# Kernel optimization log

Hardware: AMD Instinct MI355X
Metric: run time of the kernel (lower is better)

Reference implementation:

```python
import jax, jax.numpy as jnp
import numpy as np

# Config matching init_kwargs: input_shape=(C,T,H,W)=(512,32,14,14), window_size=9, n_heads=8
B, C, T, H, W = 2, 512, 32, 14, 14
N, K = 8, 9
CI = C // N              # per-head inter channels (64)
P = (K - 1) // 2         # symmetric temporal zero-pad so S == T


def setup_inputs() -> dict:
    key = jax.random.key(0)
    ks = jax.random.split(key, 7)
    s = 0.02
    return {
        "x":  jax.random.normal(ks[0], (B, C, T, H, W), jnp.float32),
        # per-head 1x1x1 conv (Linear3d) weights/biases, stacked over heads
        "Wq": jax.random.normal(ks[1], (N, CI, C), jnp.float32) * s,
        "bq": jax.random.normal(ks[2], (N, CI), jnp.float32) * s,
        "Wk": jax.random.normal(ks[3], (N, CI, C), jnp.float32) * s,
        "bk": jax.random.normal(ks[4], (N, CI), jnp.float32) * s,
        "Wv": jax.random.normal(ks[5], (N, CI, C), jnp.float32) * s,
        "bv": jax.random.normal(ks[6], (N, CI), jnp.float32) * s,
    }


def reference(x, Wq, bq, Wk, bk, Wv, bv):
    # x: (B, C, T, H, W). Dropout (p=0.25) is inference-mode identity.
    Bx, Cx, Tx, Hx, Wd = x.shape
    HW = Hx * Wd
    xf = x.reshape(Bx, Cx, Tx, HW)

    # Queries: every original frame is the center of its own window -> project x directly.
    q = jnp.einsum('bctp,nic->bnitp', xf, Wq) + bq[None, :, :, None, None]  # (B,N,ci,T,HW)

    # Keys/values on temporally zero-padded input (Pad3d gives S == T windows).
    xp = jnp.pad(xf, ((0, 0), (0, 0), (P, P), (0, 0)))  # (B,C,T+K-1,HW)
    k = jnp.einsum('bctp,nic->bnitp', xp, Wk) + bk[None, :, :, None, None]
    v = jnp.einsum('bctp,nic->bnitp', xp, Wv) + bv[None, :, :, None, None]

    # Sliding windows over padded time: window s covers padded frames s..s+K-1
    win = jnp.arange(Tx)[:, None] + jnp.arange(K)[None, :]  # (T,K)
    kw = k[:, :, :, win]  # (B,N,ci,T,K,HW)
    vw = v[:, :, :, win].reshape(Bx, N, CI, Tx, K * HW)

    # alpha[b,n,t,p,m] = sum_i q[b,n,i,t,p] * k_win[b,n,i,t,m]; softmax over keys m
    alpha = jnp.einsum('bnitp,bnitkm->bntpkm', q, kw).reshape(Bx, N, Tx, HW, K * HW)
    alpha = jax.nn.softmax(alpha, axis=-1)

    # y = alpha @ value -> (B,N,ci,T,HW); head concat is channel-major reshape
    y = jnp.einsum('bntpm,bnitm->bnitp', alpha, vw)
    z = y.reshape(Bx, Cx, Tx, Hx, Wd) + x  # residual
    return z
```

## Files before the change

### kernel.cpp

```cpp
#include <hip/hip_runtime.h>
#include <hip/hip_bf16.h>
#include <stdint.h>
#include <cstddef>

#define BB  2
#define CC  512
#define TT  32
#define HWP 196
#define NH  8
#define KWIN 9
#define CID 64
#define PPAD 4
#define TP  40
#define MTOT 12544
#define NTOT 1536
#define VSLOT 224
#define GPITCH 72
#define LOG2E 1.44269504f

typedef unsigned short u16;
typedef unsigned int   u32;
typedef __attribute__((ext_vector_type(8))) short short8;
typedef __attribute__((ext_vector_type(4))) float floatx4;

__device__ __forceinline__ u16 f2bf(float f) {
    u32 u = __float_as_uint(f);
    u32 r = (u + 0x7fffu + ((u >> 16) & 1u)) >> 16;
    return (u16)r;
}
__device__ __forceinline__ u32 pack2bf(float a, float b) {
    return (u32)f2bf(a) | ((u32)f2bf(b) << 16);
}
__device__ __forceinline__ u32 packtrunc(float a, float b) {
    return __builtin_amdgcn_perm(__float_as_uint(b), __float_as_uint(a), 0x07060302u);
}
__device__ __forceinline__ float fexp2(float x) {
    return __builtin_amdgcn_exp2f(x);
}

__global__ __launch_bounds__(256) void prep_misc(
    const float* __restrict__ Wq, const float* __restrict__ Wk,
    const float* __restrict__ Wv, u16* __restrict__ Wbf,
    const float* __restrict__ bk, const float* __restrict__ bv,
    u16* __restrict__ Kout, u16* __restrict__ Vtp)
{
    int id = blockIdx.x * 256 + threadIdx.x;
    const int wtot = NTOT * CC / 2;
    const int kper = 2 * NH * 8 * HWP * 32;
    const int vper = 2 * NH * 8 * 64 * (VSLOT/2);
    if (id < wtot) {
        int c2 = id & 255;
        int oc = id >> 8;
        int kind = oc >> 9;
        int idx = oc & 511;
        const float* src = (kind == 0 ? Wq : (kind == 1 ? Wk : Wv)) + (size_t)idx * CC + c2 * 2;
        ((u32*)Wbf)[id] = pack2bf(src[0], src[1]);
    } else if (id < wtot + kper) {
        int i = id - wtot;
        int ci2 = i & 31; i >>= 5;
        int p = i % HWP;  i /= HWP;
        int fr = i & 7;   i >>= 3;
        int head = i & 7;
        int b = i >> 3;
        int tp = fr < 4 ? fr : fr + 32;
        const float* bias = bk + head * CID + ci2 * 2;
        size_t addr = (((size_t)(b * NH + head) * TP + tp) * HWP + p) * 32 + ci2;
        ((u32*)Kout)[addr] = pack2bf(bias[0], bias[1]);
    } else if (id < wtot + kper + vper) {
        int i = id - wtot - kper;
        int s2 = i % (VSLOT/2); i /= (VSLOT/2);
        int ci = i & 63; i >>= 6;
        int fr = i & 7;  i >>= 3;
        int head = i & 7;
        int b = i >> 3;
        int tp = fr < 4 ? fr : fr + 32;
        float bias = bv[head * CID + ci];
        size_t addr = (((size_t)(b * NH + head) * TP + tp) * 64 + ci) * (VSLOT/2) + s2;
        ((u32*)Vtp)[addr] = pack2bf(bias, bias);
    }
}

__global__ __launch_bounds__(256) void transpose_x(
    const float* __restrict__ x, u16* __restrict__ xt)
{
    __shared__ float T[64 * 197];
    int bx = blockIdx.x;
    int ct = bx & 7; bx >>= 3;
    int t = bx & 31;
    int b = bx >> 5;
    int tid = threadIdx.x;
    const float* src = x + ((size_t)(b * CC + ct * 64) * TT + t) * HWP;
    for (int i = tid; i < 64 * HWP; i += 256) {
        int c = i / HWP;
        int p = i - c * HWP;
        T[c * 197 + p] = src[(size_t)c * (TT * HWP) + p];
    }
    __syncthreads();
    u16* dst = xt + (size_t)((b * TT + t) * HWP) * CC + ct * 64;
    for (int i = tid; i < HWP * 64; i += 256) {
        int p = i >> 6;
        int c = i & 63;
        dst[(size_t)p * CC + c] = f2bf(T[c * 197 + p]);
    }
}

__global__ __launch_bounds__(512) void proj_gemm2(
    const u16* __restrict__ xt, const u16* __restrict__ Wbf,
    const float* __restrict__ bq, const float* __restrict__ bk,
    const float* __restrict__ bv,
    u16* __restrict__ Qout, u16* __restrict__ Kout, u16* __restrict__ Vplain)
{
    __shared__ u16 sA[128 * GPITCH];
    __shared__ u16 sB[256 * GPITCH];

    int bx = blockIdx.x;
    int nb = bx % 6;
    int mt = bx / 6;
    int tid = threadIdx.x;
    int wave = tid >> 6, lane = tid & 63, quad = lane >> 4, l15 = lane & 15;
    int wm = wave >> 2, wn = wave & 3;
    int mbase = mt * 128 + wm * 64;
    int nbase = nb * 256 + wn * 64;

    floatx4 acc[4][4];
    #pragma unroll
    for (int ms = 0; ms < 4; ms++)
        #pragma unroll
        for (int ns = 0; ns < 4; ns++)
            acc[ms][ns] = (floatx4){0.f, 0.f, 0.f, 0.f};

    const u16* agbase = xt + (size_t)(mt * 128) * CC;
    const u16* bgbase = Wbf + (size_t)(nb * 256) * CC;

    for (int kc = 0; kc < 8; kc++) {
        __syncthreads();
        #pragma unroll
        for (int it = 0; it < 2; it++) {
            int idx = it * 512 + tid;
            int row = idx >> 3, jj = idx & 7;
            uint4 v = *(const uint4*)(agbase + (size_t)row * CC + kc * 64 + jj * 8);
            *(uint4*)&sA[row * GPITCH + jj * 8] = v;
        }
        #pragma unroll
        for (int it = 0; it < 4; it++) {
            int idx = it * 512 + tid;
            int row = idx >> 3, jj = idx & 7;
            uint4 v = *(const uint4*)(bgbase + (size_t)row * CC + kc * 64 + jj * 8);
            *(uint4*)&sB[row * GPITCH + jj * 8] = v;
        }
        __syncthreads();

        #pragma unroll
        for (int kk = 0; kk < 2; kk++) {
            short8 af[4], bf[4];
            #pragma unroll
            for (int ms = 0; ms < 4; ms++)
                af[ms] = *(const short8*)&sA[(wm * 64 + ms * 16 + l15) * GPITCH + kk * 32 + quad * 8];
            #pragma unroll
            for (int ns = 0; ns < 4; ns++)
                bf[ns] = *(const short8*)&sB[(wn * 64 + ns * 16 + l15) * GPITCH + kk * 32 + quad * 8];
            #pragma unroll
            for (int ms = 0; ms < 4; ms++)
                #pragma unroll
                for (int ns = 0; ns < 4; ns++)
                    acc[ms][ns] = __builtin_amdgcn_mfma_f32_16x16x32_bf16(
                        af[ms], bf[ns], acc[ms][ns], 0, 0, 0);
        }
    }

    float biasv[4];
    #pragma unroll
    for (int ns = 0; ns < 4; ns++) {
        int n = nbase + ns * 16 + l15;
        int kind = n >> 9;
        int idx = n & 511;
        const float* bpb = kind == 0 ? bq : (kind == 1 ? bk : bv);
        biasv[ns] = bpb[idx];
    }

    #pragma unroll
    for (int ms = 0; ms < 4; ms++) {
        #pragma unroll
        for (int r = 0; r < 4; r++) {
            int m = mbase + ms * 16 + quad * 4 + r;
            int b = m / (TT * HWP);
            int rem = m - b * (TT * HWP);
            int t = rem / HWP;
            int p = rem - t * HWP;
            #pragma unroll
            for (int ns = 0; ns < 4; ns++) {
                int n = nbase + ns * 16 + l15;
                int kind = n >> 9;
                int idx = n & 511;
                int head = idx >> 6;
                int ci = idx & 63;
                float val = acc[ms][ns][r] + biasv[ns];
                if (kind == 0) {
                    Qout[(((size_t)(b * NH + head) * TT + t) * HWP + p) * CID + ci]
                        = f2bf(val * LOG2E);
                } else if (kind == 1) {
                    Kout[(((size_t)(b * NH + head) * TP + (t + PPAD)) * HWP + p) * CID + ci]
                        = f2bf(val);
                } else {
                    Vplain[(((size_t)(b * NH + head) * TT + t) * HWP + p) * CID + ci]
                        = f2bf(val);
                }
            }
        }
    }
}

__global__ __launch_bounds__(256) void v_reformat(
    const u16* __restrict__ Vplain, u16* __restrict__ Vtp)
{
    __shared__ u16 T[HWP * 66];
    int bx = blockIdx.x;
    int t = bx & 31;
    int slab = bx >> 5;
    int tid = threadIdx.x;
    const u32* src = (const u32*)(Vplain + ((size_t)slab * TT + t) * (HWP * CID));
    for (int i = tid; i < HWP * 32; i += 256) {
        int p = i >> 5, c2 = i & 31;
        u32 v = src[i];
        T[p * 66 + c2 * 2]     = (u16)(v & 0xffffu);
        T[p * 66 + c2 * 2 + 1] = (u16)(v >> 16);
    }
    __syncthreads();
    u32* dst = (u32*)(Vtp + ((size_t)slab * TP + (t + PPAD)) * (64 * VSLOT));
    for (int i = tid; i < 64 * 98; i += 256) {
        int ci = i / 98;
        int s2 = i - ci * 98;
        int s = s2 * 2;
        int s5 = s & 31;
        int p0 = (s & ~31) | (((s5 >> 2) & 1) << 4) | ((s5 >> 3) << 2) | (s5 & 3);
        u32 lo = T[p0 * 66 + ci];
        u32 hi = T[(p0 + 1) * 66 + ci];
        dst[ci * (VSLOT / 2) + s2] = lo | (hi << 16);
    }
}

__global__ __launch_bounds__(256, 1) void attn_mfma4(
    const float* __restrict__ x,
    const u16* __restrict__ Qb, const u16* __restrict__ Kb,
    const u16* __restrict__ Vtp, float* __restrict__ zout)
{
    __shared__ float eT[HWP * 66];

    int i = blockIdx.x;
    int xcd = i & 7;
    int r = i >> 3;
    int slab = ((r >= 32) ? 8 : 0) | xcd;
    int t = r & 31;
    int b = slab >> 3, n = slab & 7;

    int tid = threadIdx.x;
    int wave = tid >> 6;
    int lane = tid & 63;
    int quad = lane >> 4, l15 = lane & 15;

    const u16* kfr0 = Kb + (size_t)slab * (TP * HWP) * CID;
    const u16* vslab = Vtp + (size_t)slab * (TP * 64 * VSLOT);
    const float tmask = (quad == 0) ? 1.0f : 0.0f;

    short8 qf[4][2];
    #pragma unroll
    for (int j = 0; j < 4; j++) {
        int qrow = (wave + 4 * j) * 16 + l15;
        qrow = qrow < HWP ? qrow : (HWP - 1);
        const u16* qp = Qb + ((size_t)(slab * TT + t) * HWP + qrow) * CID;
        qf[j][0] = *(const short8*)(qp + quad * 8);
        qf[j][1] = *(const short8*)(qp + 32 + quad * 8);
    }

    floatx4 acc[4][4];
    floatx4 accl[4];
    #pragma unroll
    for (int j = 0; j < 4; j++) {
        #pragma unroll
        for (int cg = 0; cg < 4; cg++) acc[j][cg] = (floatx4){0.f, 0.f, 0.f, 0.f};
        accl[j] = (floatx4){0.f, 0.f, 0.f, 0.f};
    }

    union { u32 w[4]; short8 s; } ones;
    ones.w[0] = 0x3F803F80u; ones.w[1] = 0x3F803F80u;
    ones.w[2] = 0x3F803F80u; ones.w[3] = 0x3F803F80u;

    #define KLOAD(c, D00, D01, D10, D11) do {                                    \
        const u16* a0_ = kfr0 + (size_t)(rbase + (c) * 32 + l15) * CID + quad * 8;\
        const u16* a1_ = a0_ + (size_t)16 * CID;                                 \
        D00 = *(const short8*)a0_;  D01 = *(const short8*)(a0_ + 32);            \
        D10 = *(const short8*)a1_;  D11 = *(const short8*)(a1_ + 32);            \
    } while (0)

    #define KLOADTAIL(D00, D01) do {                                             \
        int g_ = rbase + 192 + l15;                                              \
        g_ = g_ < (TP * HWP - 1) ? g_ : (TP * HWP - 1);                          \
        const u16* a0_ = kfr0 + (size_t)g_ * CID + quad * 8;                     \
        D00 = *(const short8*)a0_;  D01 = *(const short8*)(a0_ + 32);            \
    } while (0)

    #define VLOAD(c, D0, D1, D2, D3) do {                                        \
        const u16* v_ = vfr + l15 * VSLOT + (c) * 32 + quad * 8;                 \
        D0 = *(const short8*)v_;                                                 \
        D1 = *(const short8*)(v_ + 16 * VSLOT);                                  \
        D2 = *(const short8*)(v_ + 32 * VSLOT);                                  \
        D3 = *(const short8*)(v_ + 48 * VSLOT);                                  \
    } while (0)

    #define CHUNK_FULL(K00, K01, K10, K11, V0, V1, V2, V3)                       \
        _Pragma("unroll")                                                        \
        for (int j = 0; j < 4; j++) {                                            \
            floatx4 sc0 = (floatx4){0.f, 0.f, 0.f, 0.f};                         \
            sc0 = __builtin_amdgcn_mfma_f32_16x16x32_bf16(K00, qf[j][0], sc0, 0, 0, 0); \
            sc0 = __builtin_amdgcn_mfma_f32_16x16x32_bf16(K01, qf[j][1], sc0, 0, 0, 0); \
            floatx4 sc1 = (floatx4){0.f, 0.f, 0.f, 0.f};                         \
            sc1 = __builtin_amdgcn_mfma_f32_16x16x32_bf16(K10, qf[j][0], sc1, 0, 0, 0); \
            sc1 = __builtin_amdgcn_mfma_f32_16x16x32_bf16(K11, qf[j][1], sc1, 0, 0, 0); \
            union { u32 w[4]; short8 s; } pf;                                    \
            pf.w[0] = packtrunc(fexp2(sc0[0]), fexp2(sc0[1]));                   \
            pf.w[1] = packtrunc(fexp2(sc0[2]), fexp2(sc0[3]));                   \
            pf.w[2] = packtrunc(fexp2(sc1[0]), fexp2(sc1[1]));                   \
            pf.w[3] = packtrunc(fexp2(sc1[2]), fexp2(sc1[3]));                   \
            acc[j][0] = __builtin_amdgcn_mfma_f32_16x16x32_bf16(pf.s, V0, acc[j][0], 0, 0, 0); \
            acc[j][1] = __builtin_amdgcn_mfma_f32_16x16x32_bf16(pf.s, V1, acc[j][1], 0, 0, 0); \
            acc[j][2] = __builtin_amdgcn_mfma_f32_16x16x32_bf16(pf.s, V2, acc[j][2], 0, 0, 0); \
            acc[j][3] = __builtin_amdgcn_mfma_f32_16x16x32_bf16(pf.s, V3, acc[j][3], 0, 0, 0); \
            accl[j]   = __builtin_amdgcn_mfma_f32_16x16x32_bf16(pf.s, ones.s, accl[j], 0, 0, 0); \
        }

    #define CHUNK_TAIL(K00, K01, V0, V1, V2, V3)                                 \
        _Pragma("unroll")                                                        \
        for (int j = 0; j < 4; j++) {                                            \
            floatx4 sc0 = (floatx4){0.f, 0.f, 0.f, 0.f};                         \
            sc0 = __builtin_amdgcn_mfma_f32_16x16x32_bf16(K00, qf[j][0], sc0, 0, 0, 0); \
            sc0 = __builtin_amdgcn_mfma_f32_16x16x32_bf16(K01, qf[j][1], sc0, 0, 0, 0); \
            union { u32 w[4]; short8 s; } pf;                                    \
            pf.w[0] = packtrunc(fexp2(sc0[0]) * tmask, fexp2(sc0[1]) * tmask);   \
            pf.w[1] = packtrunc(fexp2(sc0[2]) * tmask, fexp2(sc0[3]) * tmask);   \
            pf.w[2] = 0u;                                                        \
            pf.w[3] = 0u;                                                        \
            acc[j][0] = __builtin_amdgcn_mfma_f32_16x16x32_bf16(pf.s, V0, acc[j][0], 0, 0, 0); \
            acc[j][1] = __builtin_amdgcn_mfma_f32_16x16x32_bf16(pf.s, V1, acc[j][1], 0, 0, 0); \
            acc[j][2] = __builtin_amdgcn_mfma_f32_16x16x32_bf16(pf.s, V2, acc[j][2], 0, 0, 0); \
            acc[j][3] = __builtin_amdgcn_mfma_f32_16x16x32_bf16(pf.s, V3, acc[j][3], 0, 0, 0); \
            accl[j]   = __builtin_amdgcn_mfma_f32_16x16x32_bf16(pf.s, ones.s, accl[j], 0, 0, 0); \
        }

    for (int f = 0; f < KWIN; f++) {
        int rbase = (t + f) * HWP;
        const u16* vfr = vslab + (size_t)(t + f) * (64 * VSLOT);

        short8 ka00, ka01, ka10, ka11, va0, va1, va2, va3;
        short8 kb00, kb01, kb10, kb11, vb0, vb1, vb2, vb3;
        short8 kc00, kc01, kc10, kc11, vc0, vc1, vc2, vc3;

        KLOAD(0, ka00, ka01, ka10, ka11);  VLOAD(0, va0, va1, va2, va3);
        KLOAD(1, kb00, kb01, kb10, kb11);  VLOAD(1, vb0, vb1, vb2, vb3);
        KLOAD(2, kc00, kc01, kc10, kc11);  VLOAD(2, vc0, vc1, vc2, vc3);
        CHUNK_FULL(ka00, ka01, ka10, ka11, va0, va1, va2, va3);
        KLOAD(3, ka00, ka01, ka10, ka11);  VLOAD(3, va0, va1, va2, va3);
        CHUNK_FULL(kb00, kb01, kb10, kb11, vb0, vb1, vb2, vb3);
        KLOAD(4, kb00, kb01, kb10, kb11);  VLOAD(4, vb0, vb1, vb2, vb3);
        CHUNK_FULL(kc00, kc01, kc10, kc11, vc0, vc1, vc2, vc3);
        KLOAD(5, kc00, kc01, kc10, kc11);  VLOAD(5, vc0, vc1, vc2, vc3);
        CHUNK_FULL(ka00, ka01, ka10, ka11, va0, va1, va2, va3);
        KLOADTAIL(ka00, ka01);             VLOAD(6, va0, va1, va2, va3);
        CHUNK_FULL(kb00, kb01, kb10, kb11, vb0, vb1, vb2, vb3);
        CHUNK_FULL(kc00, kc01, kc10, kc11, vc0, vc1, vc2, vc3);
        CHUNK_TAIL(ka00, ka01, va0, va1, va2, va3);
    }

    #undef KLOAD
    #undef KLOADTAIL
    #undef VLOAD
    #undef CHUNK_FULL
    #undef CHUNK_TAIL

    #pragma unroll
    for (int j = 0; j < 4; j++) {
        int tg = wave + 4 * j;
        float il[4];
        #pragma unroll
        for (int rr = 0; rr < 4; rr++) il[rr] = 1.0f / accl[j][rr];
        #pragma unroll
        for (int cg = 0; cg < 4; cg++) {
            #pragma unroll
            for (int rr = 0; rr < 4; rr++) {
                int p = tg * 16 + quad * 4 + rr;
                if (p < HWP)
                    eT[p * 66 + cg * 16 + l15] = acc[j][cg][rr] * il[rr];
            }
        }
    }
    __syncthreads();

    if (tid < HWP) {
        size_t base = ((size_t)(b * CC + n * CID) * TT + t) * HWP + tid;
        for (int ci = 0; ci < 64; ci++) {
            size_t a = base + (size_t)ci * (TT * HWP);
            zout[a] = eT[tid * 66 + ci] + x[a];
        }
    }
}

extern "C" void kernel_launch(void* const* d_in, const int* in_sizes, int n_in,
                              void* d_out, int out_size, void* d_ws, size_t ws_size,
                              hipStream_t stream) {
    const float* x  = (const float*)d_in[0];
    const float* Wq = (const float*)d_in[1];
    const float* bq = (const float*)d_in[2];
    const float* Wk = (const float*)d_in[3];
    const float* bk = (const float*)d_in[4];
    const float* Wv = (const float*)d_in[5];
    const float* bv = (const float*)d_in[6];
    float* z = (float*)d_out;

    const size_t qElems   = (size_t)BB * NH * TT * HWP * CID;
    const size_t kElems   = (size_t)BB * NH * TP * HWP * CID;
    const size_t vtpElems = (size_t)BB * NH * TP * 64 * VSLOT;

    u16* Qw  = (u16*)d_ws;
    u16* Kw  = Qw + qElems;
    u16* Vtp = Kw + kElems;
    u16* Wb  = Vtp + vtpElems;
    u16* Xt  = (u16*)d_out;
    u16* Vpl = Xt + qElems;

    {
        const int wtot = NTOT * CC / 2;
        const int kper = 2 * NH * 8 * HWP * 32;
        const int vper = 2 * NH * 8 * 64 * (VSLOT / 2);
        prep_misc<<<(wtot + kper + vper + 255) / 256, 256, 0, stream>>>(
            Wq, Wk, Wv, Wb, bk, bv, Kw, Vtp);
    }
    transpose_x<<<BB * TT * 8, 256, 0, stream>>>(x, Xt);
    proj_gemm2<<<98 * 6, 512, 0, stream>>>(Xt, Wb, bq, bk, bv, Qw, Kw, Vpl);
    v_reformat<<<BB * NH * TT, 256, 0, stream>>>(Vpl, Vtp);
    attn_mfma4<<<512, 256, 0, stream>>>(x, Qw, Kw, Vtp, z);
}
```

Baseline: 255.0 us.

## Merge prep and transpose kernels; use direct global-to-LDS loads with XOR swizzle in projection GEMM

Fuses the x transpose kernel and the weight/bias prep kernel into a single launch, which removes one kernel launch and lets the two independent jobs run concurrently. In the projection GEMM, register-staged global-to-shared copies with a padded pitch are replaced by global_load_lds direct loads into an unpadded tile, using an XOR swizzle on the source columns and on the MFMA fragment reads to avoid bank conflicts. The fused kernel reserves 50KB of shared memory for every block, including prep blocks that do not use it, which may lower occupancy for those blocks. The direct-to-LDS path depends on the per-lane swizzle mapping being correct.

Result: faster. 240.8 us (-5.6%).

```diff
diff --git a/kernel.cpp b/kernel.cpp
--- a/kernel.cpp
+++ b/kernel.cpp
@@ -15,7 +15,6 @@
 #define MTOT 12544
 #define NTOT 1536
 #define VSLOT 224
-#define GPITCH 72
 #define LOG2E 1.44269504f
 
 typedef unsigned short u16;
@@ -37,14 +36,45 @@
 __device__ __forceinline__ float fexp2(float x) {
     return __builtin_amdgcn_exp2f(x);
 }
-
-__global__ __launch_bounds__(256) void prep_misc(
+__device__ __forceinline__ void gload16(const u16* g, u16* l) {
+    __builtin_amdgcn_global_load_lds(
+        (const __attribute__((address_space(1))) u32*)g,
+        (__attribute__((address_space(3))) u32*)l, 16, 0, 0);
+}
+
+__global__ __launch_bounds__(256) void prep_transpose(
+    const float* __restrict__ x, u16* __restrict__ xt,
     const float* __restrict__ Wq, const float* __restrict__ Wk,
     const float* __restrict__ Wv, u16* __restrict__ Wbf,
     const float* __restrict__ bk, const float* __restrict__ bv,
     u16* __restrict__ Kout, u16* __restrict__ Vtp)
 {
-    int id = blockIdx.x * 256 + threadIdx.x;
+    __shared__ float T[64 * 197];
+    int bxg = blockIdx.x;
+    int tid = threadIdx.x;
+
+    if (bxg < BB * TT * 8) {
+        int bx = bxg;
+        int ct = bx & 7; bx >>= 3;
+        int t = bx & 31;
+        int b = bx >> 5;
+        const float* src = x + ((size_t)(b * CC + ct * 64) * TT + t) * HWP;
+        for (int i = tid; i < 64 * HWP; i += 256) {
+            int c = i / HWP;
+            int p = i - c * HWP;
+            T[c * 197 + p] = src[(size_t)c * (TT * HWP) + p];
+        }
+        __syncthreads();
+        u16* dst = xt + (size_t)((b * TT + t) * HWP) * CC + ct * 64;
+        for (int i = tid; i < HWP * 64; i += 256) {
+            int p = i >> 6;
+            int c = i & 63;
+            dst[(size_t)p * CC + c] = f2bf(T[c * 197 + p]);
+        }
+        return;
+    }
+
+    int id = (bxg - BB * TT * 8) * 256 + tid;
     const int wtot = NTOT * CC / 2;
     const int kper = 2 * NH * 8 * HWP * 32;
     const int vper = 2 * NH * 8 * 64 * (VSLOT/2);
@@ -80,38 +110,14 @@
     }
 }
 
-__global__ __launch_bounds__(256) void transpose_x(
-    const float* __restrict__ x, u16* __restrict__ xt)
-{
-    __shared__ float T[64 * 197];
-    int bx = blockIdx.x;
-    int ct = bx & 7; bx >>= 3;
-    int t = bx & 31;
-    int b = bx >> 5;
-    int tid = threadIdx.x;
-    const float* src = x + ((size_t)(b * CC + ct * 64) * TT + t) * HWP;
-    for (int i = tid; i < 64 * HWP; i += 256) {
-        int c = i / HWP;
-        int p = i - c * HWP;
-        T[c * 197 + p] = src[(size_t)c * (TT * HWP) + p];
-    }
-    __syncthreads();
-    u16* dst = xt + (size_t)((b * TT + t) * HWP) * CC + ct * 64;
-    for (int i = tid; i < HWP * 64; i += 256) {
-        int p = i >> 6;
-        int c = i & 63;
-        dst[(size_t)p * CC + c] = f2bf(T[c * 197 + p]);
-    }
-}
-
 __global__ __launch_bounds__(512) void proj_gemm2(
     const u16* __restrict__ xt, const u16* __restrict__ Wbf,
     const float* __restrict__ bq, const float* __restrict__ bk,
     const float* __restrict__ bv,
     u16* __restrict__ Qout, u16* __restrict__ Kout, u16* __restrict__ Vplain)
 {
-    __shared__ u16 sA[128 * GPITCH];
-    __shared__ u16 sB[256 * GPITCH];
+    __shared__ u16 sA[128 * 64];
+    __shared__ u16 sB[256 * 64];
 
     int bx = blockIdx.x;
     int nb = bx % 6;
@@ -122,6 +128,9 @@
     int mbase = mt * 128 + wm * 64;
     int nbase = nb * 256 + wn * 64;
 
+    int lr = lane >> 3;
+    int sw = ((lane & 7) * 8) ^ (lr << 3);
+
     floatx4 acc[4][4];
     #pragma unroll
     for (int ms = 0; ms < 4; ms++)
@@ -129,36 +138,35 @@
         for (int ns = 0; ns < 4; ns++)
             acc[ms][ns] = (floatx4){0.f, 0.f, 0.f, 0.f};
 
-    const u16* agbase = xt + (size_t)(mt * 128) * CC;
-    const u16* bgbase = Wbf + (size_t)(nb * 256) * CC;
+    const u16* abase = xt + (size_t)(mt * 128) * CC;
+    const u16* bbase = Wbf + (size_t)(nb * 256) * CC;
 
     for (int kc = 0; kc < 8; kc++) {
         __syncthreads();
         #pragma unroll
-        for (int it = 0; it < 2; it++) {
-            int idx = it * 512 + tid;
-            int row = idx >> 3, jj = idx & 7;
-            uint4 v = *(const uint4*)(agbase + (size_t)row * CC + kc * 64 + jj * 8);
-            *(uint4*)&sA[row * GPITCH + jj * 8] = v;
-        }
-        #pragma unroll
-        for (int it = 0; it < 4; it++) {
-            int idx = it * 512 + tid;
-            int row = idx >> 3, jj = idx & 7;
-            uint4 v = *(const uint4*)(bgbase + (size_t)row * CC + kc * 64 + jj * 8);
-            *(uint4*)&sB[row * GPITCH + jj * 8] = v;
+        for (int i = 0; i < 2; i++) {
+            int rbase = wave * 16 + i * 8;
+            gload16(abase + (size_t)(rbase + lr) * CC + kc * 64 + sw,
+                    &sA[rbase * 64]);
+        }
+        #pragma unroll
+        for (int i = 0; i < 4; i++) {
+            int rbase = wave * 32 + i * 8;
+            gload16(bbase + (size_t)(rbase + lr) * CC + kc * 64 + sw,
+                    &sB[rbase * 64]);
         }
         __syncthreads();
 
         #pragma unroll
         for (int kk = 0; kk < 2; kk++) {
+            int swr = (kk * 32 + quad * 8) ^ ((l15 & 7) << 3);
             short8 af[4], bf[4];
             #pragma unroll
             for (int ms = 0; ms < 4; ms++)
-                af[ms] = *(const short8*)&sA[(wm * 64 + ms * 16 + l15) * GPITCH + kk * 32 + quad * 8];
+                af[ms] = *(const short8*)&sA[(wm * 64 + ms * 16 + l15) * 64 + swr];
             #pragma unroll
             for (int ns = 0; ns < 4; ns++)
-                bf[ns] = *(const short8*)&sB[(wn * 64 + ns * 16 + l15) * GPITCH + kk * 32 + quad * 8];
+                bf[ns] = *(const short8*)&sB[(wn * 64 + ns * 16 + l15) * 64 + swr];
             #pragma unroll
             for (int ms = 0; ms < 4; ms++)
                 #pragma unroll
@@ -430,10 +438,10 @@
         const int wtot = NTOT * CC / 2;
         const int kper = 2 * NH * 8 * HWP * 32;
         const int vper = 2 * NH * 8 * 64 * (VSLOT / 2);
-        prep_misc<<<(wtot + kper + vper + 255) / 256, 256, 0, stream>>>(
-            Wq, Wk, Wv, Wb, bk, bv, Kw, Vtp);
-    }
-    transpose_x<<<BB * TT * 8, 256, 0, stream>>>(x, Xt);
+        const int prepBlocks = (wtot + kper + vper + 255) / 256;
+        prep_transpose<<<BB * TT * 8 + prepBlocks, 256, 0, stream>>>(
+            x, Xt, Wq, Wk, Wv, Wb, bk, bv, Kw, Vtp);
+    }
     proj_gemm2<<<98 * 6, 512, 0, stream>>>(Xt, Wb, bq, bk, bv, Qw, Kw, Vpl);
     v_reformat<<<BB * NH * TT, 256, 0, stream>>>(Vpl, Vtp);
     attn_mfma4<<<512, 256, 0, stream>>>(x, Qw, Kw, Vtp, z);
```
